# Performance work log

Measured on AMD Instinct MI355X. Metric: run time of the kernel, lower is better.

The kernel has to match this reference:

```python
import jax, jax.numpy as jnp
import numpy as np

N, E, C = 50000, 300000, 128


def _line_graph(src, dst, n):
    # PyG LineGraph(force_directed=True): line-graph node per edge; edge j -> edge i iff dst(j) == src(i)
    order = np.argsort(src, kind='stable')          # edges grouped by src node
    deg_out = np.bincount(src, minlength=n)
    ptr = np.concatenate([np.zeros(1, np.int64), np.cumsum(deg_out)])
    counts = deg_out[dst]                           # #successor edges of each edge j
    total = int(counts.sum())
    line_src = np.repeat(np.arange(src.shape[0], dtype=np.int64), counts)
    grp_start = np.repeat(ptr[dst], counts)
    cum = np.cumsum(counts)
    within = np.arange(total, dtype=np.int64) - np.repeat(cum - counts, counts)
    line_dst = order[grp_start + within]
    return np.stack([line_src, line_dst]).astype(np.int32)


def setup_inputs() -> dict:
    rng = np.random.default_rng(0)
    ei = rng.integers(0, N, size=(2, E), dtype=np.int64)
    line_ei = _line_graph(ei[0], ei[1], N)
    key = jax.random.key(0)
    k = jax.random.split(key, 6)
    s_e = float(1.0 / np.sqrt(3 * C))  # torch Linear init bound
    s_g = float(1.0 / np.sqrt(C))
    return {
        "x": jax.random.normal(k[0], (N, C), jnp.float32),
        "edge_attr": jax.random.normal(k[1], (E, C), jnp.float32),
        "W_edge": jax.random.uniform(k[2], (3 * C, C), jnp.float32, -s_e, s_e),
        "b_edge": jax.random.uniform(k[3], (C,), jnp.float32, -s_e, s_e),
        "W_gcn": jax.random.uniform(k[4], (C, C), jnp.float32, -s_g, s_g),
        "b_gcn": jnp.zeros((C,), jnp.float32),
        "edge_index": jnp.asarray(ei, dtype=jnp.int32),
        "batch": jnp.zeros((N,), jnp.int32),
        "line_edge_index": jnp.asarray(line_ei),
    }


def reference(x, edge_attr, W_edge, b_edge, W_gcn, b_gcn,
              edge_index, batch, line_edge_index):
    src, dst = edge_index[0], edge_index[1]
    # gather endpoints, concat with edge_attr, linear 3C -> C
    merged = jnp.concatenate([x[src], x[dst], edge_attr], axis=1)    # [E, 3C]
    line_x = merged @ W_edge + b_edge                                # [E, C] line-graph node feats

    # GCNConv with self loops on the line graph (line-graph nodes = original edges)
    e = line_x.shape[0]
    loops = jnp.arange(e, dtype=line_edge_index.dtype)
    row = jnp.concatenate([line_edge_index[0], loops])
    col = jnp.concatenate([line_edge_index[1], loops])
    xw = line_x @ W_gcn                                              # [E, C]
    deg = jax.ops.segment_sum(jnp.ones(row.shape, xw.dtype), col, num_segments=e)
    dinv = jnp.where(deg > 0, jax.lax.rsqrt(deg), 0.0)
    norm = dinv[row] * dinv[col]                                     # [M+E]
    out = jax.ops.segment_sum(xw[row] * norm[:, None], col, num_segments=e) + b_gcn
    return jax.nn.leaky_relu(out)  # negative_slope = 0.01 (torch default)
```

## Files before the change

### kernel.cpp

```cpp
#include <hip/hip_runtime.h>
#include <hip/hip_bf16.h>


typedef __bf16 bf16x8 __attribute__((ext_vector_type(8)));
typedef float  f32x4  __attribute__((ext_vector_type(4)));

#define C_DIM 128

__device__ __forceinline__ float bfu_lo(unsigned u) { return __uint_as_float(u << 16); }
__device__ __forceinline__ float bfu_hi(unsigned u) { return __uint_as_float(u & 0xffff0000u); }
__device__ __forceinline__ unsigned bf16_bits(float f) {
    __bf16 h = (__bf16)f;
    return (unsigned)__builtin_bit_cast(unsigned short, h);
}

__global__ void k_wcomb(const float* __restrict__ W_edge, const float* __restrict__ W_gcn,
                        const float* __restrict__ b_edge,
                        __bf16* __restrict__ Wf, float* __restrict__ b_comb) {
    int idx = blockIdx.x * 256 + threadIdx.x;
    if (idx < 384 * 128) {
        int k = idx >> 7, c = idx & 127;
        float s = 0.f;
        for (int m = 0; m < 128; ++m) s += W_edge[k * 128 + m] * W_gcn[m * 128 + c];
        int ks = k >> 5, kc8 = (k >> 3) & 3, j = k & 7;
        int col16 = c >> 4, c15 = c & 15;
        Wf[(size_t)(((ks * 8 + col16) * 64) + kc8 * 16 + c15) * 8 + j] = (__bf16)s;
    }
    if (blockIdx.x == 0 && threadIdx.x < 128) {
        int c = threadIdx.x;
        float s = 0.f;
        for (int m = 0; m < 128; ++m) s += b_edge[m] * W_gcn[m * 128 + c];
        b_comb[c] = s;
    }
}

__global__ void k_indeg(const int* __restrict__ dst, int E, int* __restrict__ indeg) {
    int e = blockIdx.x * 256 + threadIdx.x;
    if (e < E) atomicAdd(&indeg[dst[e]], 1);
}

__global__ void k_scan_bsum(const int* __restrict__ indeg, int n, int* __restrict__ bsum) {
    __shared__ int ws[16];
    int i = blockIdx.x * 1024 + threadIdx.x;
    int v = (i < n) ? indeg[i] : 0;
    int lane = threadIdx.x & 63, wid = threadIdx.x >> 6;
    for (int off = 32; off; off >>= 1) v += __shfl_down(v, off);
    if (lane == 0) ws[wid] = v;
    __syncthreads();
    if (threadIdx.x < 16) {
        int s = ws[threadIdx.x];
        for (int off = 8; off; off >>= 1) s += __shfl_down(s, off);
        if (threadIdx.x == 0) bsum[blockIdx.x] = s;
    }
}

__global__ void k_scan_top(int* __restrict__ bsum, int nb, int n, int* __restrict__ ptr) {
    int lane = threadIdx.x;
    int v = (lane < nb) ? bsum[lane] : 0;
    int incl = v;
    for (int off = 1; off < 64; off <<= 1) {
        int t = __shfl_up(incl, off);
        if (lane >= off) incl += t;
    }
    if (lane < nb) bsum[lane] = incl - v;
    if (lane == 63) ptr[n] = incl;
}

__global__ void k_scan_fin(const int* __restrict__ indeg, int n, const int* __restrict__ bsum,
                           int* __restrict__ ptr, int* __restrict__ cursor) {
    __shared__ int wsum[16];
    int i = blockIdx.x * 1024 + threadIdx.x;
    int v = (i < n) ? indeg[i] : 0;
    int lane = threadIdx.x & 63, wid = threadIdx.x >> 6;
    int incl = v;
    for (int off = 1; off < 64; off <<= 1) {
        int t = __shfl_up(incl, off);
        if (lane >= off) incl += t;
    }
    if (lane == 63) wsum[wid] = incl;
    __syncthreads();
    if (wid == 0 && lane < 16) {
        int s = wsum[lane];
        for (int off = 1; off < 16; off <<= 1) {
            int t = __shfl_up(s, off);
            if (lane >= off) s += t;
        }
        wsum[lane] = s;
    }
    __syncthreads();
    int woff = wid ? wsum[wid - 1] : 0;
    if (i < n) {
        int ex = bsum[blockIdx.x] + woff + incl - v;
        ptr[i] = ex;
        cursor[i] = ex;
    }
}

__global__ void k_place(const int* __restrict__ dst, int E,
                        int* __restrict__ cursor, int* __restrict__ adj) {
    int e = blockIdx.x * 256 + threadIdx.x;
    if (e < E) {
        int pos = atomicAdd(&cursor[dst[e]], 1);
        adj[pos] = e;
    }
}

__global__ __launch_bounds__(256) void k_p12(
    const float* __restrict__ x, const __bf16* __restrict__ Wf,
    const float* __restrict__ b_comb,
    __bf16* __restrict__ P1, __bf16* __restrict__ P2, int M) {

    __shared__ __align__(16) __bf16 As[64 * 136];

    const int tid = threadIdx.x;
    const int mbase = blockIdx.x * 64;
    const int r = tid >> 2, q = tid & 3;
    const int m_r = mbase + r;
    const int m_rc = (m_r < M) ? m_r : 0;
    const float* rp = x + (size_t)m_rc * C_DIM;

#pragma unroll
    for (int s4 = 0; s4 < 4; ++s4) {
        const float* p = rp + s4 * 32 + q * 8;
        float4 f0 = *(const float4*)p;
        float4 f1 = *(const float4*)(p + 4);
        bf16x8 h;
        h[0] = (__bf16)f0.x; h[1] = (__bf16)f0.y; h[2] = (__bf16)f0.z; h[3] = (__bf16)f0.w;
        h[4] = (__bf16)f1.x; h[5] = (__bf16)f1.y; h[6] = (__bf16)f1.z; h[7] = (__bf16)f1.w;
        int u = s4 * 4 + q;
        *(bf16x8*)&As[r * 128 + ((u ^ (r & 7)) << 3)] = h;
    }
    __syncthreads();

    const int lane = tid & 63, wid = tid >> 6;
    const int wr = wid >> 1, wc = wid & 1;
    const int kc8 = lane >> 4;
    const int arow0 = wr * 32 + (lane & 15);
    const int arow1 = arow0 + 16;
    const __bf16* wfb = Wf + ((size_t)(wc * 4) * 64 + lane) * 8;

    f32x4 acc1[2][4] = {};
    f32x4 acc2[2][4] = {};

#pragma unroll
    for (int ks = 0; ks < 4; ++ks) {
        int u = ks * 4 + kc8;
        bf16x8 a0 = *(const bf16x8*)&As[arow0 * 128 + ((u ^ (arow0 & 7)) << 3)];
        bf16x8 a1 = *(const bf16x8*)&As[arow1 * 128 + ((u ^ (arow1 & 7)) << 3)];
#pragma unroll
        for (int n = 0; n < 4; ++n) {
            bf16x8 b1 = *(const bf16x8*)&wfb[(size_t)(ks * 8 + n) * 64 * 8];
            bf16x8 b2 = *(const bf16x8*)&wfb[(size_t)((ks + 4) * 8 + n) * 64 * 8];
            acc1[0][n] = __builtin_amdgcn_mfma_f32_16x16x32_bf16(a0, b1, acc1[0][n], 0, 0, 0);
            acc1[1][n] = __builtin_amdgcn_mfma_f32_16x16x32_bf16(a1, b1, acc1[1][n], 0, 0, 0);
            acc2[0][n] = __builtin_amdgcn_mfma_f32_16x16x32_bf16(a0, b2, acc2[0][n], 0, 0, 0);
            acc2[1][n] = __builtin_amdgcn_mfma_f32_16x16x32_bf16(a1, b2, acc2[1][n], 0, 0, 0);
        }
    }

#pragma unroll
    for (int pass = 0; pass < 2; ++pass) {
        __syncthreads();
#pragma unroll
        for (int m = 0; m < 2; ++m)
#pragma unroll
            for (int j = 0; j < 4; ++j) {
                int row = wr * 32 + m * 16 + (lane >> 4) * 4 + j;
#pragma unroll
                for (int n = 0; n < 4; ++n) {
                    int c = wc * 64 + n * 16 + (lane & 15);
                    int p = ((c >> 2) & 3) * 32 + (c >> 4) * 4 + (c & 3);
                    float v = pass == 0 ? acc1[m][n][j] + b_comb[c] : acc2[m][n][j];
                    As[row * 136 + p] = (__bf16)v;
                }
            }
        __syncthreads();
        if (m_r < M) {
            __bf16* outp = (pass == 0 ? P1 : P2) + (size_t)m_r * C_DIM + q * 32;
#pragma unroll
            for (int i = 0; i < 4; ++i)
                *(bf16x8*)(outp + i * 8) = *(const bf16x8*)&As[r * 136 + q * 32 + i * 8];
        }
    }
}

__global__ __launch_bounds__(256) void k_gemm3(
    const float* __restrict__ ea, const __bf16* __restrict__ Wf,
    const __bf16* __restrict__ P1, const __bf16* __restrict__ P2,
    const int* __restrict__ src, const int* __restrict__ dst,
    const int* __restrict__ indeg, __bf16* __restrict__ xws, int E) {

    __shared__ __align__(16) __bf16 Wlds[16384];

    const int tid = threadIdx.x;
    {
        const uint4* wsrc = (const uint4*)Wf + 4096;
        uint4* wdst = (uint4*)Wlds;
#pragma unroll
        for (int i = 0; i < 8; ++i) wdst[tid + i * 256] = wsrc[tid + i * 256];
    }
    __syncthreads();

    const int wid = tid >> 6, lane = tid & 63;
    const int e15 = lane & 15, q = lane >> 4;
    const int eb0 = blockIdx.x * 128 + wid * 32;
    const int eb1 = eb0 + 16;
    if (eb0 >= E) return;
    const bool has1 = (eb1 < E);

    const int e0 = eb0 + e15;
    const int e0c = (e0 < E) ? e0 : E - 1;
    const int e1 = eb1 + e15;
    const int e1c = (e1 < E) ? e1 : E - 1;

    const int s0 = src[e0c], d0 = dst[e0c];
    const float di0 = rsqrtf(1.0f + (float)indeg[s0]);
    int s1 = s0, d1 = d0;
    float di1 = di0;
    if (has1) { s1 = src[e1c]; d1 = dst[e1c]; di1 = rsqrtf(1.0f + (float)indeg[s1]); }

    const float* ap0 = ea + (size_t)e0c * C_DIM + q * 8;
    float4 fa[8];
#pragma unroll
    for (int ks = 0; ks < 4; ++ks) {
        fa[2 * ks]     = *(const float4*)(ap0 + ks * 32);
        fa[2 * ks + 1] = *(const float4*)(ap0 + ks * 32 + 4);
    }
    uint4 hA1[4], hA2[4];
    {
        const uint4* p1 = (const uint4*)(P1 + (size_t)s0 * C_DIM + q * 32);
        const uint4* p2 = (const uint4*)(P2 + (size_t)d0 * C_DIM + q * 32);
#pragma unroll
        for (int m = 0; m < 4; ++m) { hA1[m] = p1[m]; hA2[m] = p2[m]; }
    }
    const float* ap1 = ea + (size_t)e1c * C_DIM + q * 8;
    float4 fb[8];
    if (has1) {
#pragma unroll
        for (int ks = 0; ks < 4; ++ks) {
            fb[2 * ks]     = *(const float4*)(ap1 + ks * 32);
            fb[2 * ks + 1] = *(const float4*)(ap1 + ks * 32 + 4);
        }
    }

    f32x4 acc[8] = {};
#pragma unroll
    for (int ks = 0; ks < 4; ++ks) {
        float4 f0 = fa[2 * ks], f1 = fa[2 * ks + 1];
        bf16x8 b;
        b[0] = (__bf16)f0.x; b[1] = (__bf16)f0.y; b[2] = (__bf16)f0.z; b[3] = (__bf16)f0.w;
        b[4] = (__bf16)f1.x; b[5] = (__bf16)f1.y; b[6] = (__bf16)f1.z; b[7] = (__bf16)f1.w;
#pragma unroll
        for (int n = 0; n < 8; ++n) {
            bf16x8 a = *(const bf16x8*)&Wlds[(size_t)((ks * 8 + n) * 64 + lane) * 8];
            acc[n] = __builtin_amdgcn_mfma_f32_16x16x32_bf16(a, b, acc[n], 0, 0, 0);
        }
    }

    uint4 hB1[4], hB2[4];
    if (has1) {
        const uint4* p1 = (const uint4*)(P1 + (size_t)s1 * C_DIM + q * 32);
        const uint4* p2 = (const uint4*)(P2 + (size_t)d1 * C_DIM + q * 32);
#pragma unroll
        for (int m = 0; m < 4; ++m) { hB1[m] = p1[m]; hB2[m] = p2[m]; }
    }

    if (e0 < E) {
        __bf16* op = xws + (size_t)e0 * C_DIM + q * 32;
#pragma unroll
        for (int m = 0; m < 4; ++m) {
            bf16x8 h1 = __builtin_bit_cast(bf16x8, hA1[m]);
            bf16x8 h2 = __builtin_bit_cast(bf16x8, hA2[m]);
            uint4 u;
            unsigned w[4];
#pragma unroll
            for (int hw = 0; hw < 4; ++hw) {
                int n = 2 * m + (hw >> 1);
                int j0 = (hw & 1) * 2;
                float v0 = (acc[n][j0]     + (float)h1[(hw >> 1) * 4 + j0]     + (float)h2[(hw >> 1) * 4 + j0])     * di0;
                float v1 = (acc[n][j0 + 1] + (float)h1[(hw >> 1) * 4 + j0 + 1] + (float)h2[(hw >> 1) * 4 + j0 + 1]) * di0;
                w[hw] = bf16_bits(v0) | (bf16_bits(v1) << 16);
            }
            u.x = w[0]; u.y = w[1]; u.z = w[2]; u.w = w[3];
            *(uint4*)(op + m * 8) = u;
        }
    }

    if (!has1) return;

    f32x4 acc2[8] = {};
#pragma unroll
    for (int ks = 0; ks < 4; ++ks) {
        float4 f0 = fb[2 * ks], f1 = fb[2 * ks + 1];
        bf16x8 b;
        b[0] = (__bf16)f0.x; b[1] = (__bf16)f0.y; b[2] = (__bf16)f0.z; b[3] = (__bf16)f0.w;
        b[4] = (__bf16)f1.x; b[5] = (__bf16)f1.y; b[6] = (__bf16)f1.z; b[7] = (__bf16)f1.w;
#pragma unroll
        for (int n = 0; n < 8; ++n) {
            bf16x8 a = *(const bf16x8*)&Wlds[(size_t)((ks * 8 + n) * 64 + lane) * 8];
            acc2[n] = __builtin_amdgcn_mfma_f32_16x16x32_bf16(a, b, acc2[n], 0, 0, 0);
        }
    }

    if (e1 < E) {
        __bf16* op = xws + (size_t)e1 * C_DIM + q * 32;
#pragma unroll
        for (int m = 0; m < 4; ++m) {
            bf16x8 h1 = __builtin_bit_cast(bf16x8, hB1[m]);
            bf16x8 h2 = __builtin_bit_cast(bf16x8, hB2[m]);
            uint4 u;
            unsigned w[4];
#pragma unroll
            for (int hw = 0; hw < 4; ++hw) {
                int n = 2 * m + (hw >> 1);
                int j0 = (hw & 1) * 2;
                float v0 = (acc2[n][j0]     + (float)h1[(hw >> 1) * 4 + j0]     + (float)h2[(hw >> 1) * 4 + j0])     * di1;
                float v1 = (acc2[n][j0 + 1] + (float)h1[(hw >> 1) * 4 + j0 + 1] + (float)h2[(hw >> 1) * 4 + j0 + 1]) * di1;
                w[hw] = bf16_bits(v0) | (bf16_bits(v1) << 16);
            }
            u.x = w[0]; u.y = w[1]; u.z = w[2]; u.w = w[3];
            *(uint4*)(op + m * 8) = u;
        }
    }
}

__global__ void k_agg(const __bf16* __restrict__ xws, const int* __restrict__ ptr,
                      const int* __restrict__ adj, __bf16* __restrict__ agg, int Nn) {
    int v = blockIdx.x * 4 + (threadIdx.x >> 6);
    if (v >= Nn) return;
    int c = threadIdx.x & 63;
    int b0 = ptr[v], b1 = ptr[v + 1];
    float s0 = 0.f, s1 = 0.f;
    for (int t = b0; t < b1; ++t) {
        int j = adj[t];
        unsigned u = *(const unsigned*)(xws + (size_t)j * C_DIM + c * 2);
        s0 += bfu_lo(u);
        s1 += bfu_hi(u);
    }
    unsigned o = bf16_bits(s0) | (bf16_bits(s1) << 16);
    *(unsigned*)(agg + (size_t)v * C_DIM + c * 2) = o;
}

__global__ void k_out(const __bf16* __restrict__ xws, const __bf16* __restrict__ agg,
                      const int* __restrict__ src, const int* __restrict__ indeg,
                      const float* __restrict__ b_gcn, float* __restrict__ out, int E) {
    int g = blockIdx.x * 256 + threadIdx.x;
    if (g >= E * (C_DIM / 4)) return;
    int e = g >> 5, c4 = (g & 31) * 4;
    int p4 = ((c4 >> 2) & 3) * 32 + (c4 >> 4) * 4;
    int s = src[e];
    float di = rsqrtf(1.0f + (float)indeg[s]);
    uint2 u  = *(const uint2*)(xws + (size_t)e * C_DIM + p4);
    uint2 au = *(const uint2*)(agg + (size_t)s * C_DIM + p4);
    float4 b = *(const float4*)&b_gcn[c4];
    float4 r;
    r.x = di * (bfu_lo(au.x) + bfu_lo(u.x)) + b.x;
    r.y = di * (bfu_hi(au.x) + bfu_hi(u.x)) + b.y;
    r.z = di * (bfu_lo(au.y) + bfu_lo(u.y)) + b.z;
    r.w = di * (bfu_hi(au.y) + bfu_hi(u.y)) + b.w;
    r.x = r.x > 0.f ? r.x : 0.01f * r.x;
    r.y = r.y > 0.f ? r.y : 0.01f * r.y;
    r.z = r.z > 0.f ? r.z : 0.01f * r.z;
    r.w = r.w > 0.f ? r.w : 0.01f * r.w;
    *(float4*)&out[(size_t)e * C_DIM + c4] = r;
}

extern "C" void kernel_launch(void* const* d_in, const int* in_sizes, int n_in,
                              void* d_out, int out_size, void* d_ws, size_t ws_size,
                              hipStream_t stream) {
    const float* x      = (const float*)d_in[0];
    const float* ea     = (const float*)d_in[1];
    const float* W_edge = (const float*)d_in[2];
    const float* b_edge = (const float*)d_in[3];
    const float* W_gcn  = (const float*)d_in[4];
    const float* b_gcn  = (const float*)d_in[5];
    const int*   ei     = (const int*)d_in[6];

    const int C  = in_sizes[3];
    const int Nn = in_sizes[0] / C;
    const int E  = in_sizes[1] / C;
    const int* srcp = ei;
    const int* dstp = ei + E;

    char* ws = (char*)d_ws;
    size_t off = 0;
    auto alloc = [&](size_t bytes) { size_t o = off; off = (off + bytes + 255) & ~(size_t)255; return o; };
    __bf16* Wf     = (__bf16*)(ws + alloc((size_t)384 * 128 * sizeof(__bf16)));
    float*  b_comb = (float*)(ws + alloc(128 * sizeof(float)));
    int*    indeg  = (int*)(ws + alloc((size_t)Nn * sizeof(int)));
    int*    ptr    = (int*)(ws + alloc((size_t)(Nn + 1) * sizeof(int)));
    int*    cursor = (int*)(ws + alloc((size_t)Nn * sizeof(int)));
    int*    bsum   = (int*)(ws + alloc(64 * sizeof(int)));
    int*    adj    = (int*)(ws + alloc((size_t)E * sizeof(int)));
    __bf16* P1     = (__bf16*)(ws + alloc((size_t)Nn * C * sizeof(__bf16)));
    __bf16* P2     = (__bf16*)(ws + alloc((size_t)Nn * C * sizeof(__bf16)));
    __bf16* xws    = (__bf16*)(ws + alloc((size_t)E * C * sizeof(__bf16)));
    __bf16* agg    = (__bf16*)(ws + alloc((size_t)Nn * C * sizeof(__bf16)));

    const int nb = (Nn + 1023) / 1024;

    (void)hipMemsetAsync(indeg, 0, (size_t)Nn * sizeof(int), stream);
    k_wcomb<<<192, 256, 0, stream>>>(W_edge, W_gcn, b_edge, Wf, b_comb);
    k_indeg<<<(E + 255) / 256, 256, 0, stream>>>(dstp, E, indeg);
    k_scan_bsum<<<nb, 1024, 0, stream>>>(indeg, Nn, bsum);
    k_scan_top<<<1, 64, 0, stream>>>(bsum, nb, Nn, ptr);
    k_scan_fin<<<nb, 1024, 0, stream>>>(indeg, Nn, bsum, ptr, cursor);
    k_place<<<(E + 255) / 256, 256, 0, stream>>>(dstp, E, cursor, adj);
    k_p12<<<(Nn + 63) / 64, 256, 0, stream>>>(x, Wf, b_comb, P1, P2, Nn);
    k_gemm3<<<(E + 127) / 128, 256, 0, stream>>>(ea, Wf, P1, P2, srcp, dstp, indeg, xws, E);
    k_agg<<<(Nn + 3) / 4, 256, 0, stream>>>(xws, ptr, adj, agg, Nn);
    k_out<<<(E * (C / 4) + 255) / 256, 256, 0, stream>>>(xws, agg, srcp, indeg, b_gcn, (float*)d_out, E);
}
```

Before: 240.9 us.

## Merge small setup kernels and widen gemm3 blocks to 512 threads

Folds the weight-combine kernel together with the in-degree atomic count into one launch, and the adjacency placement together with the P1/P2 projection into another, by splitting work on block index. This removes launch gaps between small, independent stages. k_gemm3 now runs 512-thread blocks covering 256 edges each and issues its edge-attribute loads before the LDS weight staging and barrier, so global latency overlaps the weight copy. The edge-count guards are dropped: with E divisible by 256 every wave has valid edges, but other sizes would rely on index clamping and the remaining e<E store checks.

```diff
diff --git a/kernel.cpp b/kernel.cpp
--- a/kernel.cpp
+++ b/kernel.cpp
@@ -14,28 +14,29 @@
     return (unsigned)__builtin_bit_cast(unsigned short, h);
 }
 
-__global__ void k_wcomb(const float* __restrict__ W_edge, const float* __restrict__ W_gcn,
-                        const float* __restrict__ b_edge,
-                        __bf16* __restrict__ Wf, float* __restrict__ b_comb) {
-    int idx = blockIdx.x * 256 + threadIdx.x;
-    if (idx < 384 * 128) {
-        int k = idx >> 7, c = idx & 127;
-        float s = 0.f;
-        for (int m = 0; m < 128; ++m) s += W_edge[k * 128 + m] * W_gcn[m * 128 + c];
-        int ks = k >> 5, kc8 = (k >> 3) & 3, j = k & 7;
-        int col16 = c >> 4, c15 = c & 15;
-        Wf[(size_t)(((ks * 8 + col16) * 64) + kc8 * 16 + c15) * 8 + j] = (__bf16)s;
-    }
-    if (blockIdx.x == 0 && threadIdx.x < 128) {
-        int c = threadIdx.x;
-        float s = 0.f;
-        for (int m = 0; m < 128; ++m) s += b_edge[m] * W_gcn[m * 128 + c];
-        b_comb[c] = s;
-    }
-}
-
-__global__ void k_indeg(const int* __restrict__ dst, int E, int* __restrict__ indeg) {
-    int e = blockIdx.x * 256 + threadIdx.x;
+__global__ void k_wcomb_indeg(const float* __restrict__ W_edge, const float* __restrict__ W_gcn,
+                              const float* __restrict__ b_edge,
+                              __bf16* __restrict__ Wf, float* __restrict__ b_comb,
+                              const int* __restrict__ dst, int E, int* __restrict__ indeg) {
+    if ((int)blockIdx.x < 192) {
+        int idx = blockIdx.x * 256 + threadIdx.x;
+        if (idx < 384 * 128) {
+            int k = idx >> 7, c = idx & 127;
+            float s = 0.f;
+            for (int m = 0; m < 128; ++m) s += W_edge[k * 128 + m] * W_gcn[m * 128 + c];
+            int ks = k >> 5, kc8 = (k >> 3) & 3, j = k & 7;
+            int col16 = c >> 4, c15 = c & 15;
+            Wf[(size_t)(((ks * 8 + col16) * 64) + kc8 * 16 + c15) * 8 + j] = (__bf16)s;
+        }
+        if (blockIdx.x == 0 && threadIdx.x < 128) {
+            int c = threadIdx.x;
+            float s = 0.f;
+            for (int m = 0; m < 128; ++m) s += b_edge[m] * W_gcn[m * 128 + c];
+            b_comb[c] = s;
+        }
+        return;
+    }
+    int e = ((int)blockIdx.x - 192) * 256 + threadIdx.x;
     if (e < E) atomicAdd(&indeg[dst[e]], 1);
 }
 
@@ -96,24 +97,26 @@
     }
 }
 
-__global__ void k_place(const int* __restrict__ dst, int E,
-                        int* __restrict__ cursor, int* __restrict__ adj) {
-    int e = blockIdx.x * 256 + threadIdx.x;
-    if (e < E) {
-        int pos = atomicAdd(&cursor[dst[e]], 1);
-        adj[pos] = e;
-    }
-}
-
-__global__ __launch_bounds__(256) void k_p12(
+__global__ __launch_bounds__(256) void k_place_p12(
+    const int* __restrict__ dst, int E, int nbPlace,
+    int* __restrict__ cursor, int* __restrict__ adj,
     const float* __restrict__ x, const __bf16* __restrict__ Wf,
     const float* __restrict__ b_comb,
     __bf16* __restrict__ P1, __bf16* __restrict__ P2, int M) {
 
     __shared__ __align__(16) __bf16 As[64 * 136];
 
+    if ((int)blockIdx.x < nbPlace) {
+        int e = blockIdx.x * 256 + threadIdx.x;
+        if (e < E) {
+            int pos = atomicAdd(&cursor[dst[e]], 1);
+            adj[pos] = e;
+        }
+        return;
+    }
+
     const int tid = threadIdx.x;
-    const int mbase = blockIdx.x * 64;
+    const int mbase = ((int)blockIdx.x - nbPlace) * 64;
     const int r = tid >> 2, q = tid & 3;
     const int m_r = mbase + r;
     const int m_rc = (m_r < M) ? m_r : 0;
@@ -184,7 +187,7 @@
     }
 }
 
-__global__ __launch_bounds__(256) void k_gemm3(
+__global__ __launch_bounds__(512, 6) void k_gemm3(
     const float* __restrict__ ea, const __bf16* __restrict__ Wf,
     const __bf16* __restrict__ P1, const __bf16* __restrict__ P2,
     const int* __restrict__ src, const int* __restrict__ dst,
@@ -193,31 +196,19 @@
     __shared__ __align__(16) __bf16 Wlds[16384];
 
     const int tid = threadIdx.x;
-    {
-        const uint4* wsrc = (const uint4*)Wf + 4096;
-        uint4* wdst = (uint4*)Wlds;
-#pragma unroll
-        for (int i = 0; i < 8; ++i) wdst[tid + i * 256] = wsrc[tid + i * 256];
-    }
-    __syncthreads();
-
     const int wid = tid >> 6, lane = tid & 63;
     const int e15 = lane & 15, q = lane >> 4;
-    const int eb0 = blockIdx.x * 128 + wid * 32;
+    const int eb0 = blockIdx.x * 256 + wid * 32;
     const int eb1 = eb0 + 16;
-    if (eb0 >= E) return;
-    const bool has1 = (eb1 < E);
-
     const int e0 = eb0 + e15;
+    const int e1 = eb1 + e15;
     const int e0c = (e0 < E) ? e0 : E - 1;
-    const int e1 = eb1 + e15;
     const int e1c = (e1 < E) ? e1 : E - 1;
 
     const int s0 = src[e0c], d0 = dst[e0c];
+    const int s1 = src[e1c], d1 = dst[e1c];
     const float di0 = rsqrtf(1.0f + (float)indeg[s0]);
-    int s1 = s0, d1 = d0;
-    float di1 = di0;
-    if (has1) { s1 = src[e1c]; d1 = dst[e1c]; di1 = rsqrtf(1.0f + (float)indeg[s1]); }
+    const float di1 = rsqrtf(1.0f + (float)indeg[s1]);
 
     const float* ap0 = ea + (size_t)e0c * C_DIM + q * 8;
     float4 fa[8];
@@ -235,13 +226,19 @@
     }
     const float* ap1 = ea + (size_t)e1c * C_DIM + q * 8;
     float4 fb[8];
-    if (has1) {
-#pragma unroll
-        for (int ks = 0; ks < 4; ++ks) {
-            fb[2 * ks]     = *(const float4*)(ap1 + ks * 32);
-            fb[2 * ks + 1] = *(const float4*)(ap1 + ks * 32 + 4);
-        }
-    }
+#pragma unroll
+    for (int ks = 0; ks < 4; ++ks) {
+        fb[2 * ks]     = *(const float4*)(ap1 + ks * 32);
+        fb[2 * ks + 1] = *(const float4*)(ap1 + ks * 32 + 4);
+    }
+
+    {
+        const uint4* wsrc = (const uint4*)Wf + 4096;
+        uint4* wdst = (uint4*)Wlds;
+#pragma unroll
+        for (int i = 0; i < 4; ++i) wdst[tid + i * 512] = wsrc[tid + i * 512];
+    }
+    __syncthreads();
 
     f32x4 acc[8] = {};
 #pragma unroll
@@ -258,7 +255,7 @@
     }
 
     uint4 hB1[4], hB2[4];
-    if (has1) {
+    {
         const uint4* p1 = (const uint4*)(P1 + (size_t)s1 * C_DIM + q * 32);
         const uint4* p2 = (const uint4*)(P2 + (size_t)d1 * C_DIM + q * 32);
 #pragma unroll
@@ -285,8 +282,6 @@
             *(uint4*)(op + m * 8) = u;
         }
     }
-
-    if (!has1) return;
 
     f32x4 acc2[8] = {};
 #pragma unroll
@@ -398,16 +393,16 @@
     __bf16* agg    = (__bf16*)(ws + alloc((size_t)Nn * C * sizeof(__bf16)));
 
     const int nb = (Nn + 1023) / 1024;
+    const int nbE = (E + 255) / 256;
+    const int nbP = (Nn + 63) / 64;
 
     (void)hipMemsetAsync(indeg, 0, (size_t)Nn * sizeof(int), stream);
-    k_wcomb<<<192, 256, 0, stream>>>(W_edge, W_gcn, b_edge, Wf, b_comb);
-    k_indeg<<<(E + 255) / 256, 256, 0, stream>>>(dstp, E, indeg);
+    k_wcomb_indeg<<<192 + nbE, 256, 0, stream>>>(W_edge, W_gcn, b_edge, Wf, b_comb, dstp, E, indeg);
     k_scan_bsum<<<nb, 1024, 0, stream>>>(indeg, Nn, bsum);
     k_scan_top<<<1, 64, 0, stream>>>(bsum, nb, Nn, ptr);
     k_scan_fin<<<nb, 1024, 0, stream>>>(indeg, Nn, bsum, ptr, cursor);
-    k_place<<<(E + 255) / 256, 256, 0, stream>>>(dstp, E, cursor, adj);
-    k_p12<<<(Nn + 63) / 64, 256, 0, stream>>>(x, Wf, b_comb, P1, P2, Nn);
-    k_gemm3<<<(E + 127) / 128, 256, 0, stream>>>(ea, Wf, P1, P2, srcp, dstp, indeg, xws, E);
+    k_place_p12<<<nbE + nbP, 256, 0, stream>>>(dstp, E, nbE, cursor, adj, x, Wf, b_comb, P1, P2, Nn);
+    k_gemm3<<<(E + 255) / 256, 512, 0, stream>>>(ea, Wf, P1, P2, srcp, dstp, indeg, xws, E);
     k_agg<<<(Nn + 3) / 4, 256, 0, stream>>>(xws, ptr, adj, agg, Nn);
     k_out<<<(E * (C / 4) + 255) / 256, 256, 0, stream>>>(xws, agg, srcp, indeg, b_gcn, (float*)d_out, E);
 }
```

After: 441.0 us. 1.83x slower.
